# Performance work log

Hardware: AMD Instinct MI355X
Metric: run time of the kernel (lower is better)

Reference implementation:

```python
import jax, jax.numpy as jnp
import numpy as np

N_NODES = 50000
N_EDGES = 800000
N_POS = 200000
NFEAT = 512
NHID = 256


def setup_inputs() -> dict:
    key = jax.random.key(0)
    ks = jax.random.split(key, 7)
    x = jax.random.normal(ks[0], (N_NODES, NFEAT), dtype=jnp.float32)
    edge_index = jax.random.randint(ks[1], (2, N_EDGES), 0, N_NODES, dtype=jnp.int32)
    edge_weight = jax.random.uniform(ks[2], (N_EDGES,), dtype=jnp.float32)
    pos_edge_index = jax.random.randint(ks[3], (2, N_POS), 0, N_NODES, dtype=jnp.int32)
    W1 = jax.random.normal(ks[4], (NFEAT, NHID), dtype=jnp.float32) * (1.0 / np.sqrt(NFEAT))
    W2 = jax.random.normal(ks[5], (NHID, NHID), dtype=jnp.float32) * (1.0 / np.sqrt(NHID))
    Wlin = jax.random.normal(ks[6], (2 * NHID, 2), dtype=jnp.float32) * (1.0 / np.sqrt(2 * NHID))
    return {"x": x, "edge_index": edge_index, "edge_weight": edge_weight,
            "pos_edge_index": pos_edge_index, "W1": W1, "W2": W2, "Wlin": Wlin}


def _gcn_conv(h, W, src, dst, edge_weight, num_nodes):
    # GCNConv(normalize=False, add_self_loops=False, bias=False):
    # out[dst] += edge_weight * (h @ W)[src]
    h = h @ W  # [N, out]
    msg = edge_weight[:, None] * h[src]  # [E, out]
    return jax.ops.segment_sum(msg, dst, num_segments=num_nodes)


def reference(x, edge_index, edge_weight, pos_edge_index, W1, W2, Wlin):
    src, dst = edge_index[0], edge_index[1]
    n = x.shape[0]
    z = _gcn_conv(x, W1, src, dst, edge_weight, n)
    z = jax.nn.relu(z)
    z = _gcn_conv(z, W2, src, dst, edge_weight, n)
    # decode: gather endpoints, concat, linear (no bias)
    h = jnp.concatenate([z[pos_edge_index[0]], z[pos_edge_index[1]]], axis=1)  # [P, 2*nhid]
    return h @ Wlin  # [P, 2]
```

## Files before the change

kernel.cpp:

```cpp
#include <hip/hip_runtime.h>

#define NHID 256
#define NFEAT 512

using short8  = __attribute__((ext_vector_type(8))) short;
using float8  = __attribute__((ext_vector_type(8))) float;
using f32x4   = __attribute__((ext_vector_type(4))) float;

__device__ __forceinline__ float b2f(unsigned short u) {
    union { float f; unsigned v; } c;
    c.v = ((unsigned)u) << 16;
    return c.f;
}
__device__ __forceinline__ unsigned short f2b(float f) {
    union { float f; unsigned u; } c;
    c.f = f;
    unsigned r = c.u + 0x7fffu + ((c.u >> 16) & 1u);
    return (unsigned short)(r >> 16);
}
__device__ __forceinline__ unsigned short f2h(float f) {
    union { _Float16 h; unsigned short u; } c;
    c.h = (_Float16)f;
    return c.u;
}
__device__ __forceinline__ float h2f(unsigned short u) {
    union { _Float16 h; unsigned short u; } c;
    c.u = u;
    return (float)c.h;
}

__device__ __forceinline__ void gload16(const void* gsrc, void* lds) {
    __builtin_amdgcn_global_load_lds((const __attribute__((address_space(1))) unsigned int*)gsrc,
                                     (__attribute__((address_space(3))) unsigned int*)lds,
                                     16, 0, 0);
}

__global__ __launch_bounds__(256) void prep_all(const float* __restrict__ W1,
                                                const float* __restrict__ W2,
                                                const float* __restrict__ Wlin,
                                                unsigned short* __restrict__ F1,
                                                float* __restrict__ WP,
                                                int* __restrict__ cursor, int M) {
    int i = blockIdx.x * blockDim.x + threadIdx.x;
    const int T1 = NFEAT * NHID;
    if (i < T1) {
        int j = i & 7, l = (i >> 3) & 63, cb = (i >> 9) & 15, t = i >> 13;
        int n = cb * 16 + (l & 15);
        int k = t * 32 + ((l >> 4) << 3) + j;
        F1[i] = f2b(W1[k * NHID + n]);
    } else if (i < T1 + NHID * 4) {
        int i3 = i - T1;
        int k = i3 >> 2, j = i3 & 3;
        const int base = (j >= 2) ? NHID : 0;
        const int col = j & 1;
        float acc = 0.f;
        for (int n = 0; n < NHID; ++n)
            acc += W2[k * NHID + n] * Wlin[(base + n) * 2 + col];
        WP[k * 4 + j] = acc;
    } else {
        int j = i - T1 - NHID * 4;
        if (j < M) cursor[j] = 0;
    }
}

__device__ __forceinline__ void gemm1_body(const float* __restrict__ x,
                                           const unsigned short* __restrict__ F1,
                                           unsigned short* __restrict__ C, int M,
                                           int brow, char* AsRaw) {
    const int tid = threadIdx.x;
    const int lane = tid & 63;
    const int wc = tid >> 6;
    const int lrow = lane & 15;
    const int lq = lane >> 4;
    const int nt = NFEAT / 32;

    int ar0 = brow + wc * 16 + (lane >> 3);
    int ar1 = ar0 + 8;
    if (ar0 >= M) ar0 = M - 1;
    if (ar1 >= M) ar1 = M - 1;
    const int aswz = ((lane & 7) ^ (lane >> 3)) * 4;
    const float* ag0 = x + (size_t)ar0 * NFEAT + aswz;
    const float* ag1 = x + (size_t)ar1 * NFEAT + aswz;
    const unsigned short* bsrc = F1 + (wc * 4) * 512 + lane * 8;

    f32x4 acc[4][4] = {};

    gload16(ag0, AsRaw + wc * 2048);
    gload16(ag1, AsRaw + wc * 2048 + 1024);
    short8 bc0 = *(const short8*)(bsrc + 0 * 512);
    short8 bc1 = *(const short8*)(bsrc + 1 * 512);
    short8 bc2 = *(const short8*)(bsrc + 2 * 512);
    short8 bc3 = *(const short8*)(bsrc + 3 * 512);
    __syncthreads();

    int p = 0;
#pragma unroll
    for (int t = 0; t < 16; ++t) {
        short8 bn0, bn1, bn2, bn3;
        if (t + 1 < nt) {
            gload16(ag0 + (t + 1) * 32, AsRaw + (p ^ 1) * 8192 + wc * 2048);
            gload16(ag1 + (t + 1) * 32, AsRaw + (p ^ 1) * 8192 + wc * 2048 + 1024);
            const unsigned short* bs_ = bsrc + (t + 1) * 8192;
            bn0 = *(const short8*)(bs_ + 0 * 512);
            bn1 = *(const short8*)(bs_ + 1 * 512);
            bn2 = *(const short8*)(bs_ + 2 * 512);
            bn3 = *(const short8*)(bs_ + 3 * 512);
        }
        short8 a[4];
#pragma unroll
        for (int m = 0; m < 4; ++m) {
            int row = m * 16 + lrow;
            const char* base = AsRaw + p * 8192 + row * 128;
            int sw = (row & 7) << 4;
            float4 f0 = *(const float4*)(base + ((lq * 32) ^ sw));
            float4 f1 = *(const float4*)(base + ((lq * 32 + 16) ^ sw));
            short8 v;
            v[0] = (short)f2b(f0.x); v[1] = (short)f2b(f0.y);
            v[2] = (short)f2b(f0.z); v[3] = (short)f2b(f0.w);
            v[4] = (short)f2b(f1.x); v[5] = (short)f2b(f1.y);
            v[6] = (short)f2b(f1.z); v[7] = (short)f2b(f1.w);
            a[m] = v;
        }
#pragma unroll
        for (int m = 0; m < 4; ++m) {
            acc[m][0] = __builtin_amdgcn_mfma_f32_16x16x32_bf16(a[m], bc0, acc[m][0], 0, 0, 0);
            acc[m][1] = __builtin_amdgcn_mfma_f32_16x16x32_bf16(a[m], bc1, acc[m][1], 0, 0, 0);
            acc[m][2] = __builtin_amdgcn_mfma_f32_16x16x32_bf16(a[m], bc2, acc[m][2], 0, 0, 0);
            acc[m][3] = __builtin_amdgcn_mfma_f32_16x16x32_bf16(a[m], bc3, acc[m][3], 0, 0, 0);
        }
        __syncthreads();
        p ^= 1;
        bc0 = bn0; bc1 = bn1; bc2 = bn2; bc3 = bn3;
    }

#pragma unroll
    for (int m = 0; m < 4; ++m)
#pragma unroll
        for (int r = 0; r < 4; ++r) {
            int row = brow + m * 16 + (lane >> 4) * 4 + r;
            if (row < M) {
#pragma unroll
                for (int n = 0; n < 4; ++n) {
                    int col = wc * 64 + n * 16 + (lane & 15);
                    C[(size_t)row * NHID + col] = f2b(acc[m][n][r]);
                }
            }
        }
}

__global__ __launch_bounds__(256) void fused_g1_hist(const float* __restrict__ x,
                                                     const unsigned short* __restrict__ F1,
                                                     unsigned short* __restrict__ C, int M,
                                                     int gblocks,
                                                     const int* __restrict__ dst,
                                                     int* __restrict__ counts,
                                                     int E, int span) {
    __shared__ char AsRaw[2 * 8192];
    if ((int)blockIdx.x < gblocks) {
        gemm1_body(x, F1, C, M, blockIdx.x * 64, AsRaw);
    } else {
        const int rank = blockIdx.x - gblocks;
        const int nrank = gridDim.x - gblocks;
        const int g = rank & 7;
        const int r8 = rank >> 3;
        const int n8 = nrank >> 3;
        const int lo = g * span;
        const int hi = min(lo + span, M);
        for (int e = r8 * blockDim.x + threadIdx.x; e < E; e += n8 * blockDim.x) {
            int d = dst[e];
            if (d >= lo && d < hi) atomicAdd(&counts[d], 1);
        }
    }
}

__global__ __launch_bounds__(256) void fused_g1_sort(const float* __restrict__ x,
                                                     const unsigned short* __restrict__ F1,
                                                     unsigned short* __restrict__ C, int M,
                                                     int gblocks, int rowbase,
                                                     const int* __restrict__ src,
                                                     const int* __restrict__ dst,
                                                     const float* __restrict__ w,
                                                     int* __restrict__ cursor,
                                                     unsigned* __restrict__ pk,
                                                     int E, int span) {
    __shared__ char AsRaw[2 * 8192];
    if ((int)blockIdx.x < gblocks) {
        gemm1_body(x, F1, C, M, (rowbase + blockIdx.x) * 64, AsRaw);
    } else {
        const int rank = blockIdx.x - gblocks;
        const int nrank = gridDim.x - gblocks;
        const int g = rank & 7;
        const int r8 = rank >> 3;
        const int n8 = nrank >> 3;
        const int lo = g * span;
        const int hi = min(lo + span, M);
        for (int e = r8 * blockDim.x + threadIdx.x; e < E; e += n8 * blockDim.x) {
            int d = dst[e];
            if (d >= lo && d < hi) {
                int pos = atomicAdd(&cursor[d], 1);
                pk[pos] = ((unsigned)f2h(w[e]) << 16) | (unsigned)src[e];
            }
        }
    }
}

__global__ __launch_bounds__(1024) void scan_local(const int* __restrict__ counts,
                                                   int* __restrict__ local,
                                                   int* __restrict__ blocksums, int n) {
    __shared__ int s[1024];
    const int tid = threadIdx.x;
    const int idx = blockIdx.x * 1024 + tid;
    int v = (idx < n) ? counts[idx] : 0;
    s[tid] = v;
    __syncthreads();
    for (int off = 1; off < 1024; off <<= 1) {
        int t = (tid >= off) ? s[tid - off] : 0;
        __syncthreads();
        s[tid] += t;
        __syncthreads();
    }
    if (idx < n) local[idx] = s[tid] - v;
    if (tid == 1023) blocksums[blockIdx.x] = s[1023];
}

__global__ __launch_bounds__(1024) void scan_sums(int* __restrict__ blocksums, int nb) {
    __shared__ int s[1024];
    const int tid = threadIdx.x;
    int v = (tid < nb) ? blocksums[tid] : 0;
    s[tid] = v;
    __syncthreads();
    for (int off = 1; off < 1024; off <<= 1) {
        int t = (tid >= off) ? s[tid - off] : 0;
        __syncthreads();
        s[tid] += t;
        __syncthreads();
    }
    if (tid < nb) blocksums[tid] = s[tid] - v;
}

__global__ __launch_bounds__(256) void scan_finalize(int* __restrict__ offsets,
                                                     int* __restrict__ cursor,
                                                     const int* __restrict__ blockoffs,
                                                     int n, int total) {
    int idx = blockIdx.x * blockDim.x + threadIdx.x;
    if (idx < n) {
        int o = offsets[idx] + blockoffs[idx >> 10];
        offsets[idx] = o;
        cursor[idx] = o;
    }
    if (idx == 0) offsets[n] = total;
}

__global__ __launch_bounds__(256) void gather1_proj(const unsigned short* __restrict__ h,
                                                    const int* __restrict__ offsets,
                                                    const unsigned* __restrict__ pk,
                                                    const float* __restrict__ WP,
                                                    float4* __restrict__ y4, int N) {
    const int lane = threadIdx.x & 63;
    const int wid = threadIdx.x >> 6;
    const int node = blockIdx.x * 4 + wid;
    if (node >= N) return;

    float wp[4][4];
#pragma unroll
    for (int i = 0; i < 4; ++i) {
        float4 r = ((const float4*)WP)[lane * 4 + i];
        wp[i][0] = r.x; wp[i][1] = r.y; wp[i][2] = r.z; wp[i][3] = r.w;
    }

    const int s0 = offsets[node];
    const int s1 = offsets[node + 1];
    float a0 = 0.f, a1 = 0.f, a2 = 0.f, a3 = 0.f;
    int i = s0;
    for (; i + 4 <= s1; i += 4) {
        unsigned qA = pk[i], qB = pk[i + 1], qC = pk[i + 2], qD = pk[i + 3];
        float wA = h2f(qA >> 16), wB = h2f(qB >> 16), wC = h2f(qC >> 16), wD = h2f(qD >> 16);
        ushort4 vA = ((const ushort4*)(h + (size_t)(qA & 0xffffu) * NHID))[lane];
        ushort4 vB = ((const ushort4*)(h + (size_t)(qB & 0xffffu) * NHID))[lane];
        ushort4 vC = ((const ushort4*)(h + (size_t)(qC & 0xffffu) * NHID))[lane];
        ushort4 vD = ((const ushort4*)(h + (size_t)(qD & 0xffffu) * NHID))[lane];
        a0 += wA * b2f(vA.x) + wB * b2f(vB.x) + wC * b2f(vC.x) + wD * b2f(vD.x);
        a1 += wA * b2f(vA.y) + wB * b2f(vB.y) + wC * b2f(vC.y) + wD * b2f(vD.y);
        a2 += wA * b2f(vA.z) + wB * b2f(vB.z) + wC * b2f(vC.z) + wD * b2f(vD.z);
        a3 += wA * b2f(vA.w) + wB * b2f(vB.w) + wC * b2f(vC.w) + wD * b2f(vD.w);
    }
    for (; i < s1; ++i) {
        unsigned q = pk[i];
        float ww = h2f(q >> 16);
        ushort4 v = ((const ushort4*)(h + (size_t)(q & 0xffffu) * NHID))[lane];
        a0 += ww * b2f(v.x);
        a1 += ww * b2f(v.y);
        a2 += ww * b2f(v.z);
        a3 += ww * b2f(v.w);
    }
    a0 = fmaxf(a0, 0.f); a1 = fmaxf(a1, 0.f);
    a2 = fmaxf(a2, 0.f); a3 = fmaxf(a3, 0.f);

    float t0 = a0 * wp[0][0] + a1 * wp[1][0] + a2 * wp[2][0] + a3 * wp[3][0];
    float t1 = a0 * wp[0][1] + a1 * wp[1][1] + a2 * wp[2][1] + a3 * wp[3][1];
    float t2 = a0 * wp[0][2] + a1 * wp[1][2] + a2 * wp[2][2] + a3 * wp[3][2];
    float t3 = a0 * wp[0][3] + a1 * wp[1][3] + a2 * wp[2][3] + a3 * wp[3][3];
#pragma unroll
    for (int off = 32; off > 0; off >>= 1) {
        t0 += __shfl_down(t0, off);
        t1 += __shfl_down(t1, off);
        t2 += __shfl_down(t2, off);
        t3 += __shfl_down(t3, off);
    }
    if (lane == 0) y4[node] = {t0, t1, t2, t3};
}

__global__ __launch_bounds__(256) void gather2_small(const float4* __restrict__ y4,
                                                     const int* __restrict__ offsets,
                                                     const unsigned* __restrict__ pk,
                                                     float2* __restrict__ za,
                                                     float2* __restrict__ zb, int N) {
    const int lane = threadIdx.x & 63;
    const int wid = threadIdx.x >> 6;
    const int grp = lane >> 4;
    const int slot = lane & 15;
    const int node = blockIdx.x * 16 + wid * 4 + grp;
    if (node >= N) return;

    const int s0 = offsets[node];
    const int s1 = offsets[node + 1];
    float x0 = 0.f, x1 = 0.f, x2 = 0.f, x3 = 0.f;
    for (int i = s0 + slot; i < s1; i += 16) {
        unsigned q = pk[i];
        float ww = h2f(q >> 16);
        float4 v = y4[q & 0xffffu];
        x0 += ww * v.x; x1 += ww * v.y; x2 += ww * v.z; x3 += ww * v.w;
    }
#pragma unroll
    for (int off = 8; off > 0; off >>= 1) {
        x0 += __shfl_xor(x0, off);
        x1 += __shfl_xor(x1, off);
        x2 += __shfl_xor(x2, off);
        x3 += __shfl_xor(x3, off);
    }
    if (slot == 0) {
        za[node] = {x0, x1};
        zb[node] = {x2, x3};
    }
}

__global__ __launch_bounds__(256) void decode_pairs(const float2* __restrict__ za,
                                                    const float2* __restrict__ zb,
                                                    const int* __restrict__ ps,
                                                    const int* __restrict__ pd,
                                                    float2* __restrict__ out, int P) {
    int p = blockIdx.x * blockDim.x + threadIdx.x;
    if (p < P) {
        float2 va = za[ps[p]];
        float2 vb = zb[pd[p]];
        out[p] = {va.x + vb.x, va.y + vb.y};
    }
}

template <bool RELU>
__global__ __launch_bounds__(256) void gemm_tiled(const float* __restrict__ A,
                                                  const float* __restrict__ B,
                                                  float* __restrict__ C,
                                                  int M, int N, int K) {
    __shared__ float As[16][65];
    __shared__ float Bs[16][64];
    const int block_row = blockIdx.x * 64;
    const int block_col = blockIdx.y * 64;
    const int tid = threadIdx.x;
    const int tx = tid & 15;
    const int ty = tid >> 4;
    float c[4][4] = {};
    for (int k0 = 0; k0 < K; k0 += 16) {
#pragma unroll
        for (int i = 0; i < 4; ++i) {
            int idx = tid + i * 256;
            int kk = idx & 15;
            int m = idx >> 4;
            int row = block_row + m;
            float v = 0.f;
            if (row < M) v = A[(long)row * K + k0 + kk];
            if (RELU) v = fmaxf(v, 0.f);
            As[kk][m] = v;
        }
#pragma unroll
        for (int i = 0; i < 4; ++i) {
            int idx = tid + i * 256;
            int n = idx & 63;
            int kk = idx >> 6;
            Bs[kk][n] = B[(long)(k0 + kk) * N + block_col + n];
        }
        __syncthreads();
#pragma unroll
        for (int kk = 0; kk < 16; ++kk) {
            float a[4], b[4];
#pragma unroll
            for (int i = 0; i < 4; ++i) a[i] = As[kk][ty * 4 + i];
#pragma unroll
            for (int j = 0; j < 4; ++j) b[j] = Bs[kk][tx * 4 + j];
#pragma unroll
            for (int i = 0; i < 4; ++i)
#pragma unroll
                for (int j = 0; j < 4; ++j) c[i][j] += a[i] * b[j];
        }
        __syncthreads();
    }
#pragma unroll
    for (int i = 0; i < 4; ++i) {
        int row = block_row + ty * 4 + i;
        if (row < M) {
            float* cp = C + (long)row * N + block_col + tx * 4;
#pragma unroll
            for (int j = 0; j < 4; ++j) cp[j] = c[i][j];
        }
    }
}

__global__ __launch_bounds__(256) void scatter_conv(const float* __restrict__ h,
                                                    const int* __restrict__ src,
                                                    const int* __restrict__ dst,
                                                    const float* __restrict__ w,
                                                    float* __restrict__ z, int E) {
    const int lane = threadIdx.x & 63;
    const int wid = threadIdx.x >> 6;
    const int nwaves = (gridDim.x * blockDim.x) >> 6;
    for (int e = blockIdx.x * 4 + wid; e < E; e += nwaves) {
        int s = src[e];
        int d = dst[e];
        float ww = w[e];
        float4 v = ((const float4*)(h + (long)s * NHID))[lane];
        float* zp = z + (long)d * NHID + lane * 4;
        atomicAdd(zp + 0, ww * v.x);
        atomicAdd(zp + 1, ww * v.y);
        atomicAdd(zp + 2, ww * v.z);
        atomicAdd(zp + 3, ww * v.w);
    }
}

__global__ __launch_bounds__(256) void decode_f(const float* __restrict__ z,
                                                const int* __restrict__ ps,
                                                const int* __restrict__ pd,
                                                const float* __restrict__ Wlin,
                                                float* __restrict__ out, int P) {
    const int lane = threadIdx.x & 63;
    const int wid = threadIdx.x >> 6;
    const int nwaves = (gridDim.x * blockDim.x) >> 6;
    float wa[8], wb[8];
#pragma unroll
    for (int i = 0; i < 8; ++i) {
        wa[i] = Wlin[(lane * 4) * 2 + i];
        wb[i] = Wlin[(NHID + lane * 4) * 2 + i];
    }
    for (int p = blockIdx.x * 4 + wid; p < P; p += nwaves) {
        int a = ps[p];
        int b = pd[p];
        float4 va = ((const float4*)(z + (long)a * NHID))[lane];
        float4 vb = ((const float4*)(z + (long)b * NHID))[lane];
        float acc0 = va.x * wa[0] + va.y * wa[2] + va.z * wa[4] + va.w * wa[6]
                   + vb.x * wb[0] + vb.y * wb[2] + vb.z * wb[4] + vb.w * wb[6];
        float acc1 = va.x * wa[1] + va.y * wa[3] + va.z * wa[5] + va.w * wa[7]
                   + vb.x * wb[1] + vb.y * wb[3] + vb.z * wb[5] + vb.w * wb[7];
#pragma unroll
        for (int off = 32; off > 0; off >>= 1) {
            acc0 += __shfl_down(acc0, off);
            acc1 += __shfl_down(acc1, off);
        }
        if (lane == 0) {
            out[(long)p * 2 + 0] = acc0;
            out[(long)p * 2 + 1] = acc1;
        }
    }
}

extern "C" void kernel_launch(void* const* d_in, const int* in_sizes, int n_in,
                              void* d_out, int out_size, void* d_ws, size_t ws_size,
                              hipStream_t stream) {
    (void)n_in; (void)out_size;
    const float* x    = (const float*)d_in[0];
    const int*   ei   = (const int*)d_in[1];
    const float* ew   = (const float*)d_in[2];
    const int*   pei  = (const int*)d_in[3];
    const float* W1   = (const float*)d_in[4];
    const float* W2   = (const float*)d_in[5];
    const float* Wlin = (const float*)d_in[6];
    float* out = (float*)d_out;

    const int E = in_sizes[2];
    const int P = in_sizes[3] / 2;
    const int M = in_sizes[0] / NFEAT;

    dim3 blk(256);
    const int* src = ei;
    const int* dst = ei + E;

    unsigned short* hA = (unsigned short*)d_ws;
    unsigned short* hB = hA + (size_t)M * NHID;
    int* offsets = (int*)(hB + (size_t)M * NHID);
    int* cursor  = offsets + (M + 1);
    unsigned* pk = (unsigned*)(cursor + M);
    int* blocksums = (int*)(pk + E);
    float2* za = (float2*)(blocksums + 1024);
    float2* zb = za + M;
    const size_t need = 2 * (size_t)M * NHID * 2 + ((size_t)2 * M + 1) * 4
                      + (size_t)E * 4 + 1024 * 4 + (size_t)M * 2 * 8;

    if (ws_size >= need && M <= 65535) {
        unsigned short* F1 = (unsigned short*)d_out;
        float* WP = (float*)((char*)d_out + (size_t)NFEAT * NHID * 2);
        float4* y4 = (float4*)hB;

        const int zt = NFEAT * NHID + NHID * 4 + M;
        prep_all<<<(zt + 255) / 256, blk, 0, stream>>>(W1, W2, Wlin, F1, WP, cursor, M);

        const int span = (M + 7) / 8;
        const int nb = (M + 1023) / 1024;
        const int g = (M + 63) / 64;
        const int g1 = g / 2;
        const int g2 = g - g1;
        const int CSRB = 1024;

        fused_g1_hist<<<g1 + CSRB, blk, 0, stream>>>(x, F1, hA, M, g1, dst, cursor, E, span);
        scan_local<<<nb, 1024, 0, stream>>>(cursor, offsets, blocksums, M);
        scan_sums<<<1, 1024, 0, stream>>>(blocksums, nb);
        scan_finalize<<<(M + 255) / 256, blk, 0, stream>>>(offsets, cursor, blocksums, M, E);
        fused_g1_sort<<<g2 + CSRB, blk, 0, stream>>>(x, F1, hA, M, g2, g1,
                                                     src, dst, ew, cursor, pk, E, span);
        gather1_proj<<<(M + 3) / 4, blk, 0, stream>>>(hA, offsets, pk, WP, y4, M);
        gather2_small<<<(M + 15) / 16, blk, 0, stream>>>(y4, offsets, pk, za, zb, M);
        decode_pairs<<<(P + 255) / 256, blk, 0, stream>>>(za, zb, pei, pei + P, (float2*)out, P);
    } else {
        float* bufA = (float*)d_ws;
        float* bufB = bufA + (size_t)M * NHID;
        const size_t zbytes = (size_t)M * NHID * sizeof(float);
        dim3 gemm_grid((M + 63) / 64, NHID / 64);
        gemm_tiled<false><<<gemm_grid, blk, 0, stream>>>(x, W1, bufA, M, NHID, NFEAT);
        hipMemsetAsync(bufB, 0, zbytes, stream);
        scatter_conv<<<2048, blk, 0, stream>>>(bufA, src, dst, ew, bufB, E);
        gemm_tiled<true><<<gemm_grid, blk, 0, stream>>>(bufB, W2, bufA, M, NHID, NHID);
        hipMemsetAsync(bufB, 0, zbytes, stream);
        scatter_conv<<<2048, blk, 0, stream>>>(bufA, src, dst, ew, bufB, E);
        decode_f<<<(P + 3) / 4, blk, 0, stream>>>(bufB, pei, pei + P, Wlin, out, P);
    }
}
```

Before: 183.3 us.

## Pre-convert x to bf16 in histogram kernel and run full GEMM from bf16

Adds a conversion pass that writes x as bf16 into workspace, co-scheduled with the dst histogram, and moves all GEMM1 row blocks into the sort kernel reading bf16 tiles. Before, GEMM1 was split across the hist and sort kernels and read fp32 x, converting in the inner loop. The new path removes per-tile conversion and halves the shared-memory tile. In exchange it adds an extra write and re-read of x as bf16 and puts the whole GEMM in one phase, so less GEMM work overlaps with the histogram.

```diff
diff --git a/kernel.cpp b/kernel.cpp
--- a/kernel.cpp
+++ b/kernel.cpp
@@ -3,9 +3,10 @@
 #define NHID 256
 #define NFEAT 512
 
-using short8  = __attribute__((ext_vector_type(8))) short;
-using float8  = __attribute__((ext_vector_type(8))) float;
-using f32x4   = __attribute__((ext_vector_type(4))) float;
+using short8   = __attribute__((ext_vector_type(8))) short;
+using ushort8v = __attribute__((ext_vector_type(8))) unsigned short;
+using float8   = __attribute__((ext_vector_type(8))) float;
+using f32x4    = __attribute__((ext_vector_type(4))) float;
 
 __device__ __forceinline__ float b2f(unsigned short u) {
     union { float f; unsigned v; } c;
@@ -63,10 +64,42 @@
     }
 }
 
-__device__ __forceinline__ void gemm1_body(const float* __restrict__ x,
-                                           const unsigned short* __restrict__ F1,
-                                           unsigned short* __restrict__ C, int M,
-                                           int brow, char* AsRaw) {
+__global__ __launch_bounds__(256) void fused_conv_hist(const float* __restrict__ x,
+                                                       unsigned short* __restrict__ xb,
+                                                       long n8, int convb,
+                                                       const int* __restrict__ dst,
+                                                       int* __restrict__ counts,
+                                                       int E, int span, int M) {
+    if ((int)blockIdx.x < convb) {
+        long i = (long)blockIdx.x * blockDim.x + threadIdx.x;
+        const long stride = (long)convb * blockDim.x;
+        for (; i < n8; i += stride) {
+            float4 v0 = ((const float4*)x)[2 * i];
+            float4 v1 = ((const float4*)x)[2 * i + 1];
+            ushort8v o;
+            o[0] = f2b(v0.x); o[1] = f2b(v0.y); o[2] = f2b(v0.z); o[3] = f2b(v0.w);
+            o[4] = f2b(v1.x); o[5] = f2b(v1.y); o[6] = f2b(v1.z); o[7] = f2b(v1.w);
+            ((ushort8v*)xb)[i] = o;
+        }
+    } else {
+        const int rank = blockIdx.x - convb;
+        const int nrank = gridDim.x - convb;
+        const int g = rank & 7;
+        const int r8 = rank >> 3;
+        const int n8b = nrank >> 3;
+        const int lo = g * span;
+        const int hi = min(lo + span, M);
+        for (int e = r8 * blockDim.x + threadIdx.x; e < E; e += n8b * blockDim.x) {
+            int d = dst[e];
+            if (d >= lo && d < hi) atomicAdd(&counts[d], 1);
+        }
+    }
+}
+
+__device__ __forceinline__ void gemm1b_body(const unsigned short* __restrict__ xb,
+                                            const unsigned short* __restrict__ F1,
+                                            unsigned short* __restrict__ C, int M,
+                                            int brow, char* AsRaw ) {
     const int tid = threadIdx.x;
     const int lane = tid & 63;
     const int wc = tid >> 6;
@@ -74,19 +107,15 @@
     const int lq = lane >> 4;
     const int nt = NFEAT / 32;
 
-    int ar0 = brow + wc * 16 + (lane >> 3);
-    int ar1 = ar0 + 8;
-    if (ar0 >= M) ar0 = M - 1;
-    if (ar1 >= M) ar1 = M - 1;
-    const int aswz = ((lane & 7) ^ (lane >> 3)) * 4;
-    const float* ag0 = x + (size_t)ar0 * NFEAT + aswz;
-    const float* ag1 = x + (size_t)ar1 * NFEAT + aswz;
+    int ar = brow + wc * 16 + (lane >> 2);
+    if (ar >= M) ar = M - 1;
+    const int aswz = ((lane & 3) ^ ((lane >> 2) & 3)) * 8;
+    const unsigned short* agp = xb + (size_t)ar * NFEAT + aswz;
     const unsigned short* bsrc = F1 + (wc * 4) * 512 + lane * 8;
 
     f32x4 acc[4][4] = {};
 
-    gload16(ag0, AsRaw + wc * 2048);
-    gload16(ag1, AsRaw + wc * 2048 + 1024);
+    gload16(agp, AsRaw + wc * 1024);
     short8 bc0 = *(const short8*)(bsrc + 0 * 512);
     short8 bc1 = *(const short8*)(bsrc + 1 * 512);
     short8 bc2 = *(const short8*)(bsrc + 2 * 512);
@@ -98,8 +127,7 @@
     for (int t = 0; t < 16; ++t) {
         short8 bn0, bn1, bn2, bn3;
         if (t + 1 < nt) {
-            gload16(ag0 + (t + 1) * 32, AsRaw + (p ^ 1) * 8192 + wc * 2048);
-            gload16(ag1 + (t + 1) * 32, AsRaw + (p ^ 1) * 8192 + wc * 2048 + 1024);
+            gload16(agp + (t + 1) * 32, AsRaw + (p ^ 1) * 4096 + wc * 1024);
             const unsigned short* bs_ = bsrc + (t + 1) * 8192;
             bn0 = *(const short8*)(bs_ + 0 * 512);
             bn1 = *(const short8*)(bs_ + 1 * 512);
@@ -110,16 +138,7 @@
 #pragma unroll
         for (int m = 0; m < 4; ++m) {
             int row = m * 16 + lrow;
-            const char* base = AsRaw + p * 8192 + row * 128;
-            int sw = (row & 7) << 4;
-            float4 f0 = *(const float4*)(base + ((lq * 32) ^ sw));
-            float4 f1 = *(const float4*)(base + ((lq * 32 + 16) ^ sw));
-            short8 v;
-            v[0] = (short)f2b(f0.x); v[1] = (short)f2b(f0.y);
-            v[2] = (short)f2b(f0.z); v[3] = (short)f2b(f0.w);
-            v[4] = (short)f2b(f1.x); v[5] = (short)f2b(f1.y);
-            v[6] = (short)f2b(f1.z); v[7] = (short)f2b(f1.w);
-            a[m] = v;
+            a[m] = *(const short8*)(AsRaw + p * 4096 + row * 64 + ((lq * 16) ^ ((row & 3) << 4)));
         }
 #pragma unroll
         for (int m = 0; m < 4; ++m) {
@@ -148,44 +167,19 @@
         }
 }
 
-__global__ __launch_bounds__(256) void fused_g1_hist(const float* __restrict__ x,
-                                                     const unsigned short* __restrict__ F1,
-                                                     unsigned short* __restrict__ C, int M,
-                                                     int gblocks,
-                                                     const int* __restrict__ dst,
-                                                     int* __restrict__ counts,
-                                                     int E, int span) {
-    __shared__ char AsRaw[2 * 8192];
+__global__ __launch_bounds__(256) void fused_g1b_sort(const unsigned short* __restrict__ xb,
+                                                      const unsigned short* __restrict__ F1,
+                                                      unsigned short* __restrict__ C, int M,
+                                                      int gblocks,
+                                                      const int* __restrict__ src,
+                                                      const int* __restrict__ dst,
+                                                      const float* __restrict__ w,
+                                                      int* __restrict__ cursor,
+                                                      unsigned* __restrict__ pk,
+                                                      int E, int span) {
+    __shared__ char AsRaw[2 * 4096];
     if ((int)blockIdx.x < gblocks) {
-        gemm1_body(x, F1, C, M, blockIdx.x * 64, AsRaw);
-    } else {
-        const int rank = blockIdx.x - gblocks;
-        const int nrank = gridDim.x - gblocks;
-        const int g = rank & 7;
-        const int r8 = rank >> 3;
-        const int n8 = nrank >> 3;
-        const int lo = g * span;
-        const int hi = min(lo + span, M);
-        for (int e = r8 * blockDim.x + threadIdx.x; e < E; e += n8 * blockDim.x) {
-            int d = dst[e];
-            if (d >= lo && d < hi) atomicAdd(&counts[d], 1);
-        }
-    }
-}
-
-__global__ __launch_bounds__(256) void fused_g1_sort(const float* __restrict__ x,
-                                                     const unsigned short* __restrict__ F1,
-                                                     unsigned short* __restrict__ C, int M,
-                                                     int gblocks, int rowbase,
-                                                     const int* __restrict__ src,
-                                                     const int* __restrict__ dst,
-                                                     const float* __restrict__ w,
-                                                     int* __restrict__ cursor,
-                                                     unsigned* __restrict__ pk,
-                                                     int E, int span) {
-    __shared__ char AsRaw[2 * 8192];
-    if ((int)blockIdx.x < gblocks) {
-        gemm1_body(x, F1, C, M, (rowbase + blockIdx.x) * 64, AsRaw);
+        gemm1b_body(xb, F1, C, M, blockIdx.x * 64, AsRaw);
     } else {
         const int rank = blockIdx.x - gblocks;
         const int nrank = gridDim.x - gblocks;
@@ -492,21 +486,21 @@
     const int* src = ei;
     const int* dst = ei + E;
 
-    unsigned short* hA = (unsigned short*)d_ws;
-    unsigned short* hB = hA + (size_t)M * NHID;
-    int* offsets = (int*)(hB + (size_t)M * NHID);
+    unsigned short* xb = (unsigned short*)d_ws;
+    unsigned short* hA = xb + (size_t)M * NFEAT;
+    float4* y4 = (float4*)(hA + (size_t)M * NHID);
+    int* offsets = (int*)(y4 + M);
     int* cursor  = offsets + (M + 1);
     unsigned* pk = (unsigned*)(cursor + M);
     int* blocksums = (int*)(pk + E);
     float2* za = (float2*)(blocksums + 1024);
     float2* zb = za + M;
-    const size_t need = 2 * (size_t)M * NHID * 2 + ((size_t)2 * M + 1) * 4
-                      + (size_t)E * 4 + 1024 * 4 + (size_t)M * 2 * 8;
+    const size_t need = (size_t)M * NFEAT * 2 + (size_t)M * NHID * 2 + (size_t)M * 16
+                      + ((size_t)2 * M + 1) * 4 + (size_t)E * 4 + 4096 + (size_t)M * 16;
 
     if (ws_size >= need && M <= 65535) {
         unsigned short* F1 = (unsigned short*)d_out;
         float* WP = (float*)((char*)d_out + (size_t)NFEAT * NHID * 2);
-        float4* y4 = (float4*)hB;
 
         const int zt = NFEAT * NHID + NHID * 4 + M;
         prep_all<<<(zt + 255) / 256, blk, 0, stream>>>(W1, W2, Wlin, F1, WP, cursor, M);
@@ -514,15 +508,15 @@
         const int span = (M + 7) / 8;
         const int nb = (M + 1023) / 1024;
         const int g = (M + 63) / 64;
-        const int g1 = g / 2;
-        const int g2 = g - g1;
+        const int CONVB = 1024;
         const int CSRB = 1024;
 
-        fused_g1_hist<<<g1 + CSRB, blk, 0, stream>>>(x, F1, hA, M, g1, dst, cursor, E, span);
+        fused_conv_hist<<<CONVB + CSRB, blk, 0, stream>>>(x, xb, (long)M * NFEAT / 8, CONVB,
+                                                          dst, cursor, E, span, M);
         scan_local<<<nb, 1024, 0, stream>>>(cursor, offsets, blocksums, M);
         scan_sums<<<1, 1024, 0, stream>>>(blocksums, nb);
         scan_finalize<<<(M + 255) / 256, blk, 0, stream>>>(offsets, cursor, blocksums, M, E);
-        fused_g1_sort<<<g2 + CSRB, blk, 0, stream>>>(x, F1, hA, M, g2, g1,
+        fused_g1b_sort<<<g + CSRB, blk, 0, stream>>>(xb, F1, hA, M, g,
                                                      src, dst, ew, cursor, pk, E, span);
         gather1_proj<<<(M + 3) / 4, blk, 0, stream>>>(hA, offsets, pk, WP, y4, M);
         gather2_small<<<(M + 15) / 16, blk, 0, stream>>>(y4, offsets, pk, za, zb, M);
```

Measured after the change: 205.1 us. 11.9% more time.

## Move histogram into prep kernel and run full GEMM1 alongside CSR sort

Applied to the files above, without the earlier changes.

The degree histogram now runs in the same launch as the weight-prep work, not alongside the first half of GEMM1. The whole GEMM1 then runs in the sort kernel, with the number of sort blocks doubled to 2048. The cursor zeroing moves to a hipMemsetAsync. This rebalances which work overlaps with the scattered atomic CSR phases and removes one launch's worth of GEMM split. The risk is that the sort kernel now carries all GEMM blocks while the hist launch has little compute to hide its atomics.

```diff
diff --git a/kernel.cpp b/kernel.cpp
--- a/kernel.cpp
+++ b/kernel.cpp
@@ -35,38 +35,52 @@
                                      16, 0, 0);
 }
 
-__global__ __launch_bounds__(256) void prep_all(const float* __restrict__ W1,
-                                                const float* __restrict__ W2,
-                                                const float* __restrict__ Wlin,
-                                                unsigned short* __restrict__ F1,
-                                                float* __restrict__ WP,
-                                                int* __restrict__ cursor, int M) {
-    int i = blockIdx.x * blockDim.x + threadIdx.x;
-    const int T1 = NFEAT * NHID;
-    if (i < T1) {
-        int j = i & 7, l = (i >> 3) & 63, cb = (i >> 9) & 15, t = i >> 13;
-        int n = cb * 16 + (l & 15);
-        int k = t * 32 + ((l >> 4) << 3) + j;
-        F1[i] = f2b(W1[k * NHID + n]);
-    } else if (i < T1 + NHID * 4) {
-        int i3 = i - T1;
-        int k = i3 >> 2, j = i3 & 3;
-        const int base = (j >= 2) ? NHID : 0;
-        const int col = j & 1;
-        float acc = 0.f;
-        for (int n = 0; n < NHID; ++n)
-            acc += W2[k * NHID + n] * Wlin[(base + n) * 2 + col];
-        WP[k * 4 + j] = acc;
+__global__ __launch_bounds__(256) void fused_prep_hist(const float* __restrict__ W1,
+                                                       const float* __restrict__ W2,
+                                                       const float* __restrict__ Wlin,
+                                                       unsigned short* __restrict__ F1,
+                                                       float* __restrict__ WP,
+                                                       int prepb,
+                                                       const int* __restrict__ dst,
+                                                       int* __restrict__ counts,
+                                                       int E, int span, int M) {
+    if ((int)blockIdx.x < prepb) {
+        int i = blockIdx.x * blockDim.x + threadIdx.x;
+        const int T1 = NFEAT * NHID;
+        if (i < T1) {
+            int j = i & 7, l = (i >> 3) & 63, cb = (i >> 9) & 15, t = i >> 13;
+            int n = cb * 16 + (l & 15);
+            int k = t * 32 + ((l >> 4) << 3) + j;
+            F1[i] = f2b(W1[k * NHID + n]);
+        } else if (i < T1 + NHID * 4) {
+            int i3 = i - T1;
+            int k = i3 >> 2, j = i3 & 3;
+            const int base = (j >= 2) ? NHID : 0;
+            const int col = j & 1;
+            float acc = 0.f;
+            for (int n = 0; n < NHID; ++n)
+                acc += W2[k * NHID + n] * Wlin[(base + n) * 2 + col];
+            WP[k * 4 + j] = acc;
+        }
     } else {
-        int j = i - T1 - NHID * 4;
-        if (j < M) cursor[j] = 0;
+        const int rank = blockIdx.x - prepb;
+        const int nrank = gridDim.x - prepb;
+        const int g = rank & 7;
+        const int r8 = rank >> 3;
+        const int n8 = nrank >> 3;
+        const int lo = g * span;
+        const int hi = min(lo + span, M);
+        for (int e = r8 * blockDim.x + threadIdx.x; e < E; e += n8 * blockDim.x) {
+            int d = dst[e];
+            if (d >= lo && d < hi) atomicAdd(&counts[d], 1);
+        }
     }
 }
 
 __device__ __forceinline__ void gemm1_body(const float* __restrict__ x,
                                            const unsigned short* __restrict__ F1,
                                            unsigned short* __restrict__ C, int M,
-                                           int brow, char* AsRaw) {
+                                           int brow, char* AsRaw ) {
     const int tid = threadIdx.x;
     const int lane = tid & 63;
     const int wc = tid >> 6;
@@ -148,35 +162,10 @@
         }
 }
 
-__global__ __launch_bounds__(256) void fused_g1_hist(const float* __restrict__ x,
+__global__ __launch_bounds__(256) void fused_g1_sort(const float* __restrict__ x,
                                                      const unsigned short* __restrict__ F1,
                                                      unsigned short* __restrict__ C, int M,
                                                      int gblocks,
-                                                     const int* __restrict__ dst,
-                                                     int* __restrict__ counts,
-                                                     int E, int span) {
-    __shared__ char AsRaw[2 * 8192];
-    if ((int)blockIdx.x < gblocks) {
-        gemm1_body(x, F1, C, M, blockIdx.x * 64, AsRaw);
-    } else {
-        const int rank = blockIdx.x - gblocks;
-        const int nrank = gridDim.x - gblocks;
-        const int g = rank & 7;
-        const int r8 = rank >> 3;
-        const int n8 = nrank >> 3;
-        const int lo = g * span;
-        const int hi = min(lo + span, M);
-        for (int e = r8 * blockDim.x + threadIdx.x; e < E; e += n8 * blockDim.x) {
-            int d = dst[e];
-            if (d >= lo && d < hi) atomicAdd(&counts[d], 1);
-        }
-    }
-}
-
-__global__ __launch_bounds__(256) void fused_g1_sort(const float* __restrict__ x,
-                                                     const unsigned short* __restrict__ F1,
-                                                     unsigned short* __restrict__ C, int M,
-                                                     int gblocks, int rowbase,
                                                      const int* __restrict__ src,
                                                      const int* __restrict__ dst,
                                                      const float* __restrict__ w,
@@ -185,7 +174,7 @@
                                                      int E, int span) {
     __shared__ char AsRaw[2 * 8192];
     if ((int)blockIdx.x < gblocks) {
-        gemm1_body(x, F1, C, M, (rowbase + blockIdx.x) * 64, AsRaw);
+        gemm1_body(x, F1, C, M, blockIdx.x * 64, AsRaw);
     } else {
         const int rank = blockIdx.x - gblocks;
         const int nrank = gridDim.x - gblocks;
@@ -508,22 +497,20 @@
         float* WP = (float*)((char*)d_out + (size_t)NFEAT * NHID * 2);
         float4* y4 = (float4*)hB;
 
-        const int zt = NFEAT * NHID + NHID * 4 + M;
-        prep_all<<<(zt + 255) / 256, blk, 0, stream>>>(W1, W2, Wlin, F1, WP, cursor, M);
-
         const int span = (M + 7) / 8;
         const int nb = (M + 1023) / 1024;
         const int g = (M + 63) / 64;
-        const int g1 = g / 2;
-        const int g2 = g - g1;
-        const int CSRB = 1024;
-
-        fused_g1_hist<<<g1 + CSRB, blk, 0, stream>>>(x, F1, hA, M, g1, dst, cursor, E, span);
+        const int CSRB = 2048;
+        const int prepb = (NFEAT * NHID + NHID * 4 + 255) / 256;
+
+        hipMemsetAsync(cursor, 0, (size_t)M * sizeof(int), stream);
+        fused_prep_hist<<<prepb + 1024, blk, 0, stream>>>(W1, W2, Wlin, F1, WP, prepb,
+                                                          dst, cursor, E, span, M);
         scan_local<<<nb, 1024, 0, stream>>>(cursor, offsets, blocksums, M);
         scan_sums<<<1, 1024, 0, stream>>>(blocksums, nb);
         scan_finalize<<<(M + 255) / 256, blk, 0, stream>>>(offsets, cursor, blocksums, M, E);
-        fused_g1_sort<<<g2 + CSRB, blk, 0, stream>>>(x, F1, hA, M, g2, g1,
-                                                     src, dst, ew, cursor, pk, E, span);
+        fused_g1_sort<<<g + CSRB, blk, 0, stream>>>(x, F1, hA, M, g,
+                                                    src, dst, ew, cursor, pk, E, span);
         gather1_proj<<<(M + 3) / 4, blk, 0, stream>>>(hA, offsets, pk, WP, y4, M);
         gather2_small<<<(M + 15) / 16, blk, 0, stream>>>(y4, offsets, pk, za, zb, M);
         decode_pairs<<<(P + 255) / 256, blk, 0, stream>>>(za, zb, pei, pei + P, (float2*)out, P);
```

After: 186.9 us. About the same (+2.0%).
